# Kernel tuning notes

Hardware: AMD Instinct MI355X
Metric: run time of the kernel (lower is better)

The kernel has to match this reference:

```python
import jax, jax.numpy as jnp
import numpy as np

B, L, C = 64, 64, 16          # batch, seq_len, chars per word
V, CV = 100000, 100           # word vocab, char vocab
EMB, CHD = 300, 64            # word emb dim, char emb dim
N_HIGHWAY, N_ATTN = 2, 2
D = EMB + 3 * 50              # highway_dim = 450


def setup_inputs() -> dict:
    ks = jax.random.split(jax.random.key(0), 16)
    word_emb = jax.random.normal(ks[6], (V, EMB), jnp.float32) * 0.01
    word_emb = word_emb.at[0].set(0.0)  # padding_idx row zeroed
    return {
        "q1": jax.random.randint(ks[0], (B, L), 0, V),
        "q2": jax.random.randint(ks[1], (B, L), 0, V),
        "q1_len": jax.random.randint(ks[2], (B,), 1, L + 1),
        "q2_len": jax.random.randint(ks[3], (B,), 1, L + 1),
        "q1_char": jax.random.randint(ks[4], (B, L, C), 0, CV),
        "q2_char": jax.random.randint(ks[5], (B, L, C), 0, CV),
        "word_emb": word_emb,
        "char_emb": jax.random.normal(ks[7], (CV, CHD), jnp.float32) * 0.1,
        "conv_w3": jax.random.normal(ks[8], (50, CHD, 3), jnp.float32) / np.sqrt(CHD * 3),
        "conv_b3": jnp.zeros((50,), jnp.float32),
        "conv_w4": jax.random.normal(ks[9], (50, CHD, 4), jnp.float32) / np.sqrt(CHD * 4),
        "conv_b4": jnp.zeros((50,), jnp.float32),
        "conv_w5": jax.random.normal(ks[10], (50, CHD, 5), jnp.float32) / np.sqrt(CHD * 5),
        "conv_b5": jnp.zeros((50,), jnp.float32),
        "hw_w": jax.random.normal(ks[11], (D, D), jnp.float32) / np.sqrt(D),
        "hw_b": jnp.zeros((D,), jnp.float32),
        "attn_w": jax.random.normal(ks[12], (N_ATTN, 3 * D), jnp.float32) / np.sqrt(3 * D),
        "attn_b": jnp.zeros((N_ATTN,), jnp.float32),
    }


def _char_features(qc, emb, convs):
    # qc: [B, T, C] int -> [B, T, 150]
    Bq, T, Cc = qc.shape
    e = emb[qc.reshape(-1, Cc)].transpose(0, 2, 1)  # [B*T, CHD, C]
    outs = []
    for w, b in convs:
        h = jax.lax.conv_general_dilated(e, w, (1,), 'VALID',
                                         dimension_numbers=('NCH', 'OIH', 'NCH'))
        h = jax.nn.relu(h + b[None, :, None])
        outs.append(jnp.max(h, axis=2))  # max over char positions
    return jnp.concatenate(outs, axis=-1).reshape(Bq, T, -1)


def _highway(x, w, b):
    # NB: original reuses the SAME linear for transform and gate (bug-faithful)
    y = x @ w.T + b
    g = jax.nn.sigmoid(y)
    return g * jax.nn.relu(y) + (1.0 - g) * x


def _self_attn(x, mask, w, b):
    # Exact decomposition of Linear(concat(x_i, x_j, x_i*x_j)) -> scalar:
    # score[b,i,j] = x_i.w1 + x_j.w2 + sum_d x_i x_j w3 + b
    d = x.shape[-1]
    w1, w2, w3 = w[:d], w[d:2 * d], w[2 * d:]
    scores = ((x @ w1)[:, :, None] + (x @ w2)[:, None, :]
              + jnp.einsum('bid,bjd->bij', x * w3, x) + b)
    # original masked_fill uses -1e-09 (not -1e9) -- reproduce faithfully
    logits = jnp.where(mask[:, None, :], scores, jnp.float32(-1e-9))
    attn = jax.nn.softmax(logits, axis=-1)
    return jnp.einsum('bij,bjd->bid', attn, x)


def _branch(q, q_char, q_len, word_emb, char_emb, convs, hw_w, hw_b, attn_w, attn_b):
    mask = jnp.arange(L)[None, :] < q_len[:, None]
    x = jnp.concatenate([word_emb[q], _char_features(q_char, char_emb, convs)], axis=-1)
    for _ in range(N_HIGHWAY):
        x = _highway(x, hw_w, hw_b)
    att = x
    for i in range(N_ATTN):
        att = _self_attn(x, mask, attn_w[i], attn_b[i])
        x = att + x
    return att


def reference(q1, q2, q1_len, q2_len, q1_char, q2_char, word_emb, char_emb,
              conv_w3, conv_b3, conv_w4, conv_b4, conv_w5, conv_b5,
              hw_w, hw_b, attn_w, attn_b):
    convs = [(conv_w3, conv_b3), (conv_w4, conv_b4), (conv_w5, conv_b5)]
    a1 = _branch(q1, q1_char, q1_len, word_emb, char_emb, convs, hw_w, hw_b, attn_w, attn_b)
    a2 = _branch(q2, q2_char, q2_len, word_emb, char_emb, convs, hw_w, hw_b, attn_w, attn_b)
    return (a1, a2)
```

## Files before the change

### kernel.cpp

```cpp
#include <hip/hip_runtime.h>
#include <math.h>

#define B   64
#define L   64
#define C   16
#define CHD 64
#define EMB 300
#define D   450
#define DP  480
#define NT  (B*L)
#define NBH 128

typedef short bf16x8 __attribute__((ext_vector_type(8)));
typedef float f32x4  __attribute__((ext_vector_type(4)));
typedef float f32x2  __attribute__((ext_vector_type(2)));
typedef unsigned short ushort_t;
typedef ushort_t us4 __attribute__((ext_vector_type(4)));

#define MFMA16 __builtin_amdgcn_mfma_f32_16x16x32_bf16

#define WPF_N (10 * 10 * 512)
#define WBF_N (32 * 15 * 512)
#define XFRAG 30720

__device__ inline float wave_sum(float v) {
#pragma unroll
    for (int o = 32; o; o >>= 1) v += __shfl_xor(v, o, 64);
    return v;
}
__device__ inline ushort_t f2b(float f) {
    union { float f; unsigned u; } c; c.f = f;
    unsigned r = c.u + 0x7FFFu + ((c.u >> 16) & 1u);
    return (ushort_t)(r >> 16);
}

__global__ __launch_bounds__(256) void prep_kernel(
    const float* __restrict__ W,
    const float* __restrict__ w3, const float* __restrict__ b3,
    const float* __restrict__ w4, const float* __restrict__ b4,
    const float* __restrict__ w5, const float* __restrict__ b5,
    const float* __restrict__ char_emb,
    ushort_t* __restrict__ Wb16F, ushort_t* __restrict__ WpadF,
    float* __restrict__ bias160, ushort_t* __restrict__ ceb16)
{
    int idx = blockIdx.x * 256 + threadIdx.x;
    if (idx < WBF_N) {
        const int e = idx & 7, l = (idx >> 3) & 63, t = idx >> 9;
        const int ks = t % 15, nt = t / 15;
        const int ln = l & 15, q = l >> 4;
        const int n = nt * 16 + ln, k = ks * 32 + q * 8 + e;
        float v = (n < D && k < D) ? W[(size_t)n * D + k] : 0.f;
        Wb16F[idx] = f2b(v);
        return;
    }
    idx -= WBF_N;
    if (idx < WPF_N) {
        const int e = idx & 7, l = (idx >> 3) & 63, t = idx >> 9;
        const int ks = t % 10, nt = t / 10;
        const int ln = l & 15, q = l >> 4;
        const int f = nt * 16 + ln;
        const int kd = ks * 32 + q * 8 + e;
        const int k = kd >> 6, d = kd & 63;
        float v = 0.f;
        if (f < 50)       { if (k < 3) v = w3[f * 192 + d * 3 + k]; }
        else if (f < 100) { if (k < 4) v = w4[(f - 50) * 256 + d * 4 + k]; }
        else if (f < 150) { v = w5[(f - 100) * 320 + d * 5 + k]; }
        WpadF[idx] = f2b(v);
        return;
    }
    idx -= WPF_N;
    if (idx < 160) {
        bias160[idx] = (idx < 50) ? b3[idx] : (idx < 100) ? b4[idx - 50]
                     : (idx < 150) ? b5[idx - 100] : 0.f;
    } else if (idx < 160 + 100 * 64) {
        int i = idx - 160;
        ceb16[i] = f2b(char_emb[i]);
    }
}

#define ESS 72
#define EST (20 * ESS)
#define XTS1 488

__global__ __launch_bounds__(256) void embed_conv_kernel(
    const int* __restrict__ q1, const int* __restrict__ q2,
    const int* __restrict__ q1c, const int* __restrict__ q2c,
    const float* __restrict__ word_emb, const ushort_t* __restrict__ ceb16,
    const ushort_t* __restrict__ WpadF, const float* __restrict__ bias160,
    float* __restrict__ xout, ushort_t* __restrict__ xbF)
{
    __shared__ ushort_t es[8 * EST];
    __shared__ ushort_t Xt[8 * XTS1];

    const int tid  = threadIdx.x;
    const int wv   = tid >> 6;
    const int lane = tid & 63;
    const int ln   = lane & 15, quad = lane >> 4;
    const int bx   = blockIdx.x;
    const int tokbase = ((bx & 7) * 128 + (bx >> 3)) * 8;

#pragma unroll
    for (int i = 0; i < 4; ++i) {
        int c = tid + i * 256;
        int row = c >> 3, part = c & 7;
        int tl = row >> 4, cr = row & 15;
        int gtok   = tokbase + tl;
        int branch = gtok >> 12;
        int tokl   = gtok & (NT - 1);
        int cid    = (branch ? q2c : q1c)[tokl * C + cr];
        *(bf16x8*)&es[tl * EST + cr * ESS + part * 8] =
            *(const bf16x8*)&ceb16[cid * 64 + part * 8];
    }
    {
        int tl = tid >> 5, rr = (tid >> 3) & 3, part = tid & 7;
        bf16x8 z = {0, 0, 0, 0, 0, 0, 0, 0};
        *(bf16x8*)&es[tl * EST + (16 + rr) * ESS + part * 8] = z;
    }

#pragma unroll 1
    for (int c = tid; c < 8 * 75; c += 256) {
        const int t  = c / 75, d4 = c - t * 75;
        const int tok    = tokbase + t;
        const int branch = tok >> 12;
        const int tokl   = tok & (NT - 1);
        const int w      = (branch ? q2 : q1)[tokl];
        const float4 v = *(const float4*)(word_emb + (size_t)w * EMB + d4 * 4);
        float* dst = xout + (size_t)tok * D + d4 * 4;
        *(f32x2*)dst       = (f32x2){v.x, v.y};
        *(f32x2*)(dst + 2) = (f32x2){v.z, v.w};
        us4 pk = { f2b(v.x), f2b(v.y), f2b(v.z), f2b(v.w) };
        *(us4*)&Xt[t * XTS1 + d4 * 4] = pk;
    }
    if (tid < 240) {
        const int t = tid / 30, k = tid - t * 30;
        Xt[t * XTS1 + D + k] = 0;
    }
    __syncthreads();

    const int t0 = wv * 2, t1 = t0 + 1;
    f32x4 acc[2][10];
#pragma unroll
    for (int t = 0; t < 2; ++t)
#pragma unroll
        for (int nt = 0; nt < 10; ++nt) acc[t][nt] = (f32x4){0.f, 0.f, 0.f, 0.f};

#pragma unroll 1
    for (int ks = 0; ks < 10; ++ks) {
        const int kk   = ks * 32 + quad * 8;
        const int arow = kk >> 6, aoff = kk & 63;
        bf16x8 a0 = *(const bf16x8*)&es[t0 * EST + (ln + arow) * ESS + aoff];
        bf16x8 a1 = *(const bf16x8*)&es[t1 * EST + (ln + arow) * ESS + aoff];
#pragma unroll
        for (int nt = 0; nt < 10; ++nt) {
            bf16x8 bf = *(const bf16x8*)&WpadF[(size_t)((nt * 10 + ks) << 9) + lane * 8];
            acc[0][nt] = MFMA16(a0, bf, acc[0][nt], 0, 0, 0);
            acc[1][nt] = MFMA16(a1, bf, acc[1][nt], 0, 0, 0);
        }
    }
    __syncthreads();

    float* smf = (float*)es;
#pragma unroll
    for (int t = 0; t < 2; ++t) {
        const int tloc = t0 + t;
#pragma unroll
        for (int nt = 0; nt < 10; ++nt) {
            const int f  = nt * 16 + ln;
            const int Pf = (f < 50) ? 14 : (f < 100) ? 13 : 12;
            float m = -1e30f;
#pragma unroll
            for (int r = 0; r < 4; ++r) {
                const int p = quad * 4 + r;
                if (p < Pf) m = fmaxf(m, acc[t][nt][r]);
            }
            m = fmaxf(m, __shfl_xor(m, 16, 64));
            m = fmaxf(m, __shfl_xor(m, 32, 64));
            if (quad == 0) smf[tloc * 160 + f] = fmaxf(0.f, m + bias160[f]);
        }
    }
    __syncthreads();
#pragma unroll 1
    for (int c = tid; c < 8 * 150; c += 256) {
        const int t = c / 150, f = c - t * 150;
        const float rv = smf[t * 160 + f];
        xout[(size_t)(tokbase + t) * D + EMB + f] = rv;
        Xt[t * XTS1 + EMB + f] = f2b(rv);
    }
    __syncthreads();

    {
        const int tile = tokbase >> 4, half = (tokbase >> 3) & 1;
#pragma unroll 1
        for (int c = tid; c < 480; c += 256) {
            const int ksl = c >> 5, s = c & 31;
            const int q = s >> 3, tl = s & 7;
            const int l = q * 16 + half * 8 + tl;
            bf16x8 v = *(const bf16x8*)&Xt[tl * XTS1 + ksl * 32 + q * 8];
            *(bf16x8*)&xbF[((size_t)(tile * 15 + ksl) * 64 + l) * 8] = v;
        }
    }
}

#define HLS 72

__global__ __launch_bounds__(256, 4) void highway_mfma_kernel(
    const ushort_t* __restrict__ xbFi, const float* __restrict__ xf32,
    const ushort_t* __restrict__ Wb16F, const float* __restrict__ bvec,
    float* __restrict__ out, ushort_t* __restrict__ xbFo)
{
    __shared__ ushort_t Xl[64 * HLS];

    const int bx = blockIdx.x;
    const int cx = bx & 7, rr = bx >> 3;
    const int my = cx * 16 + (rr & 15);
    const int mx = rr >> 4;

    const int tid  = threadIdx.x;
    const int wv   = tid >> 6;
    const int lane = tid & 63;
    const int wm = wv >> 1, wn = wv & 1;
    const int m0 = my * 64 + wm * 32;
    const int n0 = mx * 64 + wn * 32;
    const int lm = lane & 15, quad = lane >> 4;

    const int tA0 = my * 4 + wm * 2;
    const ushort_t* ax0 = xbFi + (size_t)(tA0 * 15) * 512 + lane * 8;
    const ushort_t* ax1 = ax0 + 15 * 512;
    const int ntg0 = mx * 4 + wn * 2;
    const ushort_t* bw0 = Wb16F + (size_t)(ntg0 * 15) * 512 + lane * 8;
    const ushort_t* bw1 = bw0 + 15 * 512;

    f32x4 acc[2][2];
#pragma unroll
    for (int i = 0; i < 2; ++i)
#pragma unroll
        for (int j = 0; j < 2; ++j) acc[i][j] = (f32x4){0.f, 0.f, 0.f, 0.f};

#pragma unroll 3
    for (int ks = 0; ks < 15; ++ks) {
        bf16x8 a0 = *(const bf16x8*)(ax0 + ks * 512);
        bf16x8 a1 = *(const bf16x8*)(ax1 + ks * 512);
        bf16x8 b0 = *(const bf16x8*)(bw0 + ks * 512);
        bf16x8 b1 = *(const bf16x8*)(bw1 + ks * 512);
        acc[0][0] = MFMA16(a0, b0, acc[0][0], 0, 0, 0);
        acc[0][1] = MFMA16(a0, b1, acc[0][1], 0, 0, 0);
        acc[1][0] = MFMA16(a1, b0, acc[1][0], 0, 0, 0);
        acc[1][1] = MFMA16(a1, b1, acc[1][1], 0, 0, 0);
    }

#pragma unroll
    for (int nt = 0; nt < 2; ++nt) {
        const int n  = n0 + nt * 16 + lm;
        const int nl = wn * 32 + nt * 16 + lm;
        const bool nval = (n < D);
        const float bv = nval ? bvec[n] : 0.f;
#pragma unroll
        for (int mt = 0; mt < 2; ++mt) {
#pragma unroll
            for (int r = 0; r < 4; ++r) {
                const int m  = m0 + mt * 16 + quad * 4 + r;
                const int ml = wm * 32 + mt * 16 + quad * 4 + r;
                float y = acc[mt][nt][r] + bv;
                float g = 1.f / (1.f + __expf(-y));
                float o = 0.f;
                if (nval) {
                    float xo = xf32[(size_t)m * D + n];
                    o = g * fmaxf(y, 0.f) + (1.f - g) * xo;
                    out[(size_t)m * D + n] = o;
                }
                Xl[ml * HLS + nl] = f2b(nval ? o : 0.f);
            }
        }
    }
    __syncthreads();

#pragma unroll 1
    for (int c = tid; c < 512; c += 256) {
        const int fi = c >> 6, l = c & 63;
        const int tl = fi >> 1, ksl = fi & 1;
        const int ksg = mx * 2 + ksl;
        if (ksg < 15) {
            const int lnp = l & 15, qp = l >> 4;
            bf16x8 v = *(const bf16x8*)&Xl[(tl * 16 + lnp) * HLS + ksl * 32 + qp * 8];
            *(bf16x8*)&xbFo[((size_t)((my * 4 + tl) * 15 + ksg) * 64 + l) * 8] = v;
        }
    }
}

#define PXS 496

__global__ __launch_bounds__(256) void attn_prep_kernel(
    const float* __restrict__ xf32, const float* __restrict__ attn_w, int layer,
    ushort_t* __restrict__ xw3F, ushort_t* __restrict__ xTF,
    float* __restrict__ s1g, float* __restrict__ s2g)
{
    __shared__ ushort_t Xs[16 * PXS];
    __shared__ ushort_t Xw3s[16 * PXS];

    const int bx  = blockIdx.x;
    const int wid = (bx & 7) * 64 + (bx >> 3);
    const int bh  = wid >> 2, jq = wid & 3;
    const int tid = threadIdx.x;
    const int wv  = tid >> 6;
    const int lane = tid & 63;
    const size_t tok0 = (size_t)bh * 64 + jq * 16;

    const float* wb = attn_w + (size_t)layer * 3 * D;
    const float* w3 = wb + 2 * D;

#pragma unroll 1
    for (int c = tid; c < 16 * 60; c += 256) {
        const int j  = c / 60, k8 = c - j * 60;
        const int k0 = k8 * 8;
        const float* xr = xf32 + (tok0 + j) * D;
        bf16x8 xv, pv;
#pragma unroll
        for (int t = 0; t < 8; ++t) {
            const int k = k0 + t;
            const float x = (k < D) ? xr[k] : 0.f;
            xv[t] = (short)f2b(x);
            pv[t] = (short)f2b((k < D) ? x * w3[k] : 0.f);
        }
        *(bf16x8*)&Xs[j * PXS + k0]   = xv;
        *(bf16x8*)&Xw3s[j * PXS + k0] = pv;
    }

#pragma unroll 1
    for (int rr = 0; rr < 4; ++rr) {
        const int j = wv * 4 + rr;
        const float* xr = xf32 + (tok0 + j) * D;
        float a1 = 0.f, a2 = 0.f;
#pragma unroll
        for (int t = 0; t < 8; ++t) {
            const int k = lane + t * 64;
            if (k < D) {
                float xv = xr[k];
                a1 = fmaf(xv, wb[k], a1);
                a2 = fmaf(xv, wb[D + k], a2);
            }
        }
        a1 = wave_sum(a1);
        a2 = wave_sum(a2);
        if (lane == 0) { s1g[tok0 + j] = a1; s2g[tok0 + j] = a2; }
    }
    __syncthreads();

#pragma unroll 1
    for (int c = tid; c < 960; c += 256) {
        const int ks = c >> 6, l = c & 63;
        const int lnp = l & 15, qp = l >> 4;
        bf16x8 w = *(const bf16x8*)&Xw3s[lnp * PXS + ks * 32 + qp * 8];
        *(bf16x8*)&xw3F[(size_t)bh * XFRAG + ((jq * 15 + ks) * 64 + l) * 8] = w;
    }

    {
        const int half = jq >> 1, q0 = (jq & 1) * 2;
#pragma unroll 1
        for (int c = tid; c < 960; c += 256) {
            const int dt = c >> 5, s = c & 31;
            const int qp = q0 + (s >> 4), lnp = s & 15;
            const int d  = dt * 16 + lnp;
            const int jb = (qp & 1) * 8;
            bf16x8 v;
#pragma unroll
            for (int e = 0; e < 8; ++e) v[e] = (short)Xs[(jb + e) * PXS + d];
            *(bf16x8*)&xTF[(size_t)bh * XFRAG + ((dt * 2 + half) * 64 + qp * 16 + lnp) * 8] = v;
        }
    }
}

#define ALS 72

template <bool RES_EMIT>
__global__ __launch_bounds__(256) void attn_fused_kernel(
    const float* __restrict__ xf32,
    const ushort_t* __restrict__ xF, const ushort_t* __restrict__ xw3F,
    const ushort_t* __restrict__ xTF,
    const float* __restrict__ s1g, const float* __restrict__ s2g,
    const int* __restrict__ q1_len, const int* __restrict__ q2_len,
    const float* __restrict__ attn_b, int layer,
    float* __restrict__ outf, ushort_t* __restrict__ xbFo)
{
    __shared__ float    sc[16][68];
    __shared__ ushort_t Al[16 * ALS];
    __shared__ ushort_t At[RES_EMIT ? 16 * XTS1 : 8];

    const int bx  = blockIdx.x;
    const int wid = (bx & 7) * 64 + (bx >> 3);
    const int bh  = wid >> 2, iq = wid & 3;
    const int branch = bh >> 6, b = bh & 63;
    const int tid  = threadIdx.x;
    const int wv   = tid >> 6;
    const int lane = tid & 63;
    const int ln   = lane & 15, quad = lane >> 4;
    const int i0   = iq * 16;

    if (RES_EMIT) {
        for (int c = tid; c < 480; c += 256) {
            const int t = c / 30, k = c - t * 30;
            At[t * XTS1 + D + k] = 0;
        }
    }

    const ushort_t* xa = xF   + (size_t)bh * XFRAG + (iq * 15 * 64 + lane) * 8;
    const ushort_t* xb = xw3F + (size_t)bh * XFRAG + (wv * 15 * 64 + lane) * 8;

    f32x4 qa0 = (f32x4){0.f, 0.f, 0.f, 0.f};
    f32x4 qa1 = (f32x4){0.f, 0.f, 0.f, 0.f};
#pragma unroll
    for (int ks = 0; ks < 14; ks += 2) {
        bf16x8 a0 = *(const bf16x8*)(xa + ks * 512);
        bf16x8 b0 = *(const bf16x8*)(xb + ks * 512);
        bf16x8 a1 = *(const bf16x8*)(xa + ks * 512 + 512);
        bf16x8 b1 = *(const bf16x8*)(xb + ks * 512 + 512);
        qa0 = MFMA16(a0, b0, qa0, 0, 0, 0);
        qa1 = MFMA16(a1, b1, qa1, 0, 0, 0);
    }
    {
        bf16x8 a  = *(const bf16x8*)(xa + 14 * 512);
        bf16x8 bq = *(const bf16x8*)(xb + 14 * 512);
        qa0 = MFMA16(a, bq, qa0, 0, 0, 0);
    }
    f32x4 qacc = qa0 + qa1;

    const int   len  = (branch ? q2_len : q1_len)[b];
    const float bias = attn_b[layer];
    const int   j    = wv * 16 + ln;
    const float s2v  = s2g[bh * 64 + j];
#pragma unroll
    for (int reg = 0; reg < 4; ++reg) {
        const int i = i0 + quad * 4 + reg;
        float v = qacc[reg] + s1g[bh * 64 + i] + s2v + bias;
        if (j >= len) v = -1e-9f;
        sc[quad * 4 + reg][j] = v;
    }
    __syncthreads();

#pragma unroll
    for (int rr = 0; rr < 4; ++rr) {
        const int r = wv * 4 + rr;
        float v = sc[r][lane];
        float m = v;
#pragma unroll
        for (int o = 32; o; o >>= 1) m = fmaxf(m, __shfl_xor(m, o, 64));
        float ev = __expf(v - m);
        float sm = ev;
#pragma unroll
        for (int o = 32; o; o >>= 1) sm += __shfl_xor(sm, o, 64);
        Al[r * ALS + lane] = f2b(ev * (1.f / sm));
    }
    __syncthreads();

    const ushort_t* xTb = xTF + (size_t)bh * XFRAG + lane * 8;
    bf16x8 af0 = *(const bf16x8*)&Al[ln * ALS + quad * 8];
    bf16x8 af1 = *(const bf16x8*)&Al[ln * ALS + quad * 8 + 32];

#pragma unroll 2
    for (int dt = wv; dt < 30; dt += 4) {
        bf16x8 b0 = *(const bf16x8*)(xTb + dt * 1024);
        bf16x8 b1 = *(const bf16x8*)(xTb + dt * 1024 + 512);
        f32x4 acc = (f32x4){0.f, 0.f, 0.f, 0.f};
        acc = MFMA16(af0, b0, acc, 0, 0, 0);
        acc = MFMA16(af1, b1, acc, 0, 0, 0);

        const int d = dt * 16 + ln;
        if (d < D) {
#pragma unroll
            for (int reg = 0; reg < 4; ++reg) {
                const int i = i0 + quad * 4 + reg;
                float v = acc[reg];
                if (RES_EMIT) v += xf32[((size_t)bh * 64 + i) * D + d];
                outf[((size_t)bh * 64 + i) * D + d] = v;
                if (RES_EMIT)
                    At[(quad * 4 + reg) * XTS1 + d] = f2b(v);
            }
        }
    }

    if (RES_EMIT) {
        __syncthreads();
#pragma unroll 1
        for (int c = tid; c < 960; c += 256) {
            const int ksl = c >> 6, l = c & 63;
            const int lnp = l & 15, qp = l >> 4;
            bf16x8 v = *(const bf16x8*)&At[lnp * XTS1 + ksl * 32 + qp * 8];
            *(bf16x8*)&xbFo[((size_t)((bh * 4 + iq) * 15 + ksl) * 64 + l) * 8] = v;
        }
    }
}

extern "C" void kernel_launch(void* const* d_in, const int* in_sizes, int n_in,
                              void* d_out, int out_size, void* d_ws, size_t ws_size,
                              hipStream_t stream) {
    const int*   q1       = (const int*)  d_in[0];
    const int*   q2       = (const int*)  d_in[1];
    const int*   q1_len   = (const int*)  d_in[2];
    const int*   q2_len   = (const int*)  d_in[3];
    const int*   q1c      = (const int*)  d_in[4];
    const int*   q2c      = (const int*)  d_in[5];
    const float* word_emb = (const float*)d_in[6];
    const float* char_emb = (const float*)d_in[7];
    const float* w3       = (const float*)d_in[8];
    const float* b3       = (const float*)d_in[9];
    const float* w4       = (const float*)d_in[10];
    const float* b4       = (const float*)d_in[11];
    const float* w5       = (const float*)d_in[12];
    const float* b5       = (const float*)d_in[13];
    const float* hw_w     = (const float*)d_in[14];
    const float* hw_b     = (const float*)d_in[15];
    const float* attn_w   = (const float*)d_in[16];
    const float* attn_b   = (const float*)d_in[17];
    float* out = (float*)d_out;

    float*    buf0    = (float*)d_ws;
    float*    buf1    = buf0 + (size_t)2 * NT * D;
    float*    bias160 = buf1 + (size_t)2 * NT * D;
    ushort_t* xbFa    = (ushort_t*)(bias160 + 160);
    ushort_t* xbFb    = xbFa + (size_t)2 * NT * DP;
    ushort_t* Wb16F   = xbFb + (size_t)2 * NT * DP;
    ushort_t* WpadF   = Wb16F + (size_t)WBF_N;
    ushort_t* ceb16   = WpadF + (size_t)WPF_N;
    ushort_t* xw3F    = ceb16 + (size_t)100 * 64;
    ushort_t* xTF     = xw3F + (size_t)NBH * XFRAG;
    float*    s1g     = (float*)(xTF + (size_t)NBH * XFRAG);
    float*    s2g     = s1g + (size_t)2 * NT;

    prep_kernel<<<(WBF_N + WPF_N + 160 + 100 * 64 + 255) / 256, 256, 0, stream>>>(
        hw_w, w3, b3, w4, b4, w5, b5, char_emb, Wb16F, WpadF, bias160, ceb16);
    embed_conv_kernel<<<1024, 256, 0, stream>>>(q1, q2, q1c, q2c, word_emb, ceb16,
                                                WpadF, bias160, buf0, xbFa);

    highway_mfma_kernel<<<1024, 256, 0, stream>>>(xbFa, buf0, Wb16F, hw_b, buf1, xbFb);
    highway_mfma_kernel<<<1024, 256, 0, stream>>>(xbFb, buf1, Wb16F, hw_b, buf0, xbFa);

    attn_prep_kernel<<<512, 256, 0, stream>>>(buf0, attn_w, 0, xw3F, xTF, s1g, s2g);
    attn_fused_kernel<true><<<512, 256, 0, stream>>>(
        buf0, xbFa, xw3F, xTF, s1g, s2g, q1_len, q2_len, attn_b, 0, buf1, xbFb);

    attn_prep_kernel<<<512, 256, 0, stream>>>(buf1, attn_w, 1, xw3F, xTF, s1g, s2g);
    attn_fused_kernel<false><<<512, 256, 0, stream>>>(
        buf1, xbFb, xw3F, xTF, s1g, s2g, q1_len, q2_len, attn_b, 1, out, nullptr);
}
```

Measured before the change: 323.3 us.

## Fuse second highway with attention prep and attention layer with next prep

Merges the second highway layer with the layer-0 attention preparation (s1/s2 dot products, x*w3 and transposed fragments), and merges layer-0 attention with layer-1 preparation. This cuts the launch count from 7 to 5 and removes fp32 activation round-trips through global memory between kernels. In exchange the fused highway kernel runs only 512 blocks and each wave does 8 N-tiles over the full K, so it has less parallelism than the 1024-block highway kernel. It also uses more shared memory for the fp32 staging buffers.

```diff
diff --git a/kernel.cpp b/kernel.cpp
--- a/kernel.cpp
+++ b/kernel.cpp
@@ -22,6 +22,9 @@
 #define WPF_N (10 * 10 * 512)
 #define WBF_N (32 * 15 * 512)
 #define XFRAG 30720
+
+#define XFS 456
+#define XSS 488
 
 __device__ inline float wave_sum(float v) {
 #pragma unroll
@@ -80,7 +83,6 @@
 
 #define ESS 72
 #define EST (20 * ESS)
-#define XTS1 488
 
 __global__ __launch_bounds__(256) void embed_conv_kernel(
     const int* __restrict__ q1, const int* __restrict__ q2,
@@ -90,7 +92,7 @@
     float* __restrict__ xout, ushort_t* __restrict__ xbF)
 {
     __shared__ ushort_t es[8 * EST];
-    __shared__ ushort_t Xt[8 * XTS1];
+    __shared__ ushort_t Xt[8 * XSS];
 
     const int tid  = threadIdx.x;
     const int wv   = tid >> 6;
@@ -129,11 +131,11 @@
         *(f32x2*)dst       = (f32x2){v.x, v.y};
         *(f32x2*)(dst + 2) = (f32x2){v.z, v.w};
         us4 pk = { f2b(v.x), f2b(v.y), f2b(v.z), f2b(v.w) };
-        *(us4*)&Xt[t * XTS1 + d4 * 4] = pk;
+        *(us4*)&Xt[t * XSS + d4 * 4] = pk;
     }
     if (tid < 240) {
         const int t = tid / 30, k = tid - t * 30;
-        Xt[t * XTS1 + D + k] = 0;
+        Xt[t * XSS + D + k] = 0;
     }
     __syncthreads();
 
@@ -184,7 +186,7 @@
         const int t = c / 150, f = c - t * 150;
         const float rv = smf[t * 160 + f];
         xout[(size_t)(tokbase + t) * D + EMB + f] = rv;
-        Xt[t * XTS1 + EMB + f] = f2b(rv);
+        Xt[t * XSS + EMB + f] = f2b(rv);
     }
     __syncthreads();
 
@@ -195,7 +197,7 @@
             const int ksl = c >> 5, s = c & 31;
             const int q = s >> 3, tl = s & 7;
             const int l = q * 16 + half * 8 + tl;
-            bf16x8 v = *(const bf16x8*)&Xt[tl * XTS1 + ksl * 32 + q * 8];
+            bf16x8 v = *(const bf16x8*)&Xt[tl * XSS + ksl * 32 + q * 8];
             *(bf16x8*)&xbF[((size_t)(tile * 15 + ksl) * 64 + l) * 8] = v;
         }
     }
@@ -287,70 +289,108 @@
     }
 }
 
-#define PXS 496
-
-__global__ __launch_bounds__(256) void attn_prep_kernel(
-    const float* __restrict__ xf32, const float* __restrict__ attn_w, int layer,
+__global__ __launch_bounds__(256) void highway2_prep_kernel(
+    const ushort_t* __restrict__ xbFi, const float* __restrict__ xf32in,
+    const ushort_t* __restrict__ Wb16F, const float* __restrict__ bvec,
+    const float* __restrict__ attn_w,
+    float* __restrict__ outf, ushort_t* __restrict__ xbFo,
     ushort_t* __restrict__ xw3F, ushort_t* __restrict__ xTF,
     float* __restrict__ s1g, float* __restrict__ s2g)
 {
-    __shared__ ushort_t Xs[16 * PXS];
-    __shared__ ushort_t Xw3s[16 * PXS];
+    __shared__ float    Xf[16 * XFS];
+    __shared__ ushort_t Xs[16 * XSS];
 
     const int bx  = blockIdx.x;
     const int wid = (bx & 7) * 64 + (bx >> 3);
     const int bh  = wid >> 2, jq = wid & 3;
+    const int tt  = wid;
+    const int m0  = tt * 16;
     const int tid = threadIdx.x;
     const int wv  = tid >> 6;
     const int lane = tid & 63;
-    const size_t tok0 = (size_t)bh * 64 + jq * 16;
-
-    const float* wb = attn_w + (size_t)layer * 3 * D;
+    const int ln = lane & 15, quad = lane >> 4;
+
+    if (tid < 480) {
+        const int t = tid / 30, k = tid - t * 30;
+        Xs[t * XSS + D + k] = 0;
+    }
+
+    const ushort_t* ax = xbFi + (size_t)(tt * 15) * 512 + lane * 8;
+    f32x4 acc[8];
+#pragma unroll
+    for (int t = 0; t < 8; ++t) acc[t] = (f32x4){0.f, 0.f, 0.f, 0.f};
+
+#pragma unroll 1
+    for (int ks = 0; ks < 15; ++ks) {
+        bf16x8 a = *(const bf16x8*)(ax + ks * 512);
+#pragma unroll
+        for (int t = 0; t < 8; ++t) {
+            const int nt = wv * 8 + t;
+            if (nt < 30) {
+                bf16x8 b = *(const bf16x8*)&Wb16F[(size_t)(nt * 15 + ks) * 512 + lane * 8];
+                acc[t] = MFMA16(a, b, acc[t], 0, 0, 0);
+            }
+        }
+    }
+
+#pragma unroll
+    for (int t = 0; t < 8; ++t) {
+        const int nt = wv * 8 + t;
+        if (nt >= 30) continue;
+        const int n = nt * 16 + ln;
+        const bool nval = (n < D);
+        const float bv = nval ? bvec[n] : 0.f;
+#pragma unroll
+        for (int reg = 0; reg < 4; ++reg) {
+            const int i = quad * 4 + reg;
+            float y = acc[t][reg] + bv;
+            float g = 1.f / (1.f + __expf(-y));
+            if (nval) {
+                float xo = xf32in[(size_t)(m0 + i) * D + n];
+                float o = g * fmaxf(y, 0.f) + (1.f - g) * xo;
+                outf[(size_t)(m0 + i) * D + n] = o;
+                Xf[i * XFS + n] = o;
+                Xs[i * XSS + n] = f2b(o);
+            }
+        }
+    }
+    __syncthreads();
+
+    const float* wb = attn_w;
     const float* w3 = wb + 2 * D;
-
-#pragma unroll 1
-    for (int c = tid; c < 16 * 60; c += 256) {
-        const int j  = c / 60, k8 = c - j * 60;
-        const int k0 = k8 * 8;
-        const float* xr = xf32 + (tok0 + j) * D;
-        bf16x8 xv, pv;
-#pragma unroll
-        for (int t = 0; t < 8; ++t) {
-            const int k = k0 + t;
-            const float x = (k < D) ? xr[k] : 0.f;
-            xv[t] = (short)f2b(x);
-            pv[t] = (short)f2b((k < D) ? x * w3[k] : 0.f);
-        }
-        *(bf16x8*)&Xs[j * PXS + k0]   = xv;
-        *(bf16x8*)&Xw3s[j * PXS + k0] = pv;
-    }
 
 #pragma unroll 1
     for (int rr = 0; rr < 4; ++rr) {
         const int j = wv * 4 + rr;
-        const float* xr = xf32 + (tok0 + j) * D;
         float a1 = 0.f, a2 = 0.f;
 #pragma unroll
         for (int t = 0; t < 8; ++t) {
             const int k = lane + t * 64;
             if (k < D) {
-                float xv = xr[k];
+                float xv = Xf[j * XFS + k];
                 a1 = fmaf(xv, wb[k], a1);
                 a2 = fmaf(xv, wb[D + k], a2);
             }
         }
         a1 = wave_sum(a1);
         a2 = wave_sum(a2);
-        if (lane == 0) { s1g[tok0 + j] = a1; s2g[tok0 + j] = a2; }
-    }
-    __syncthreads();
+        if (lane == 0) { s1g[m0 + j] = a1; s2g[m0 + j] = a2; }
+    }
 
 #pragma unroll 1
     for (int c = tid; c < 960; c += 256) {
         const int ks = c >> 6, l = c & 63;
         const int lnp = l & 15, qp = l >> 4;
-        bf16x8 w = *(const bf16x8*)&Xw3s[lnp * PXS + ks * 32 + qp * 8];
-        *(bf16x8*)&xw3F[(size_t)bh * XFRAG + ((jq * 15 + ks) * 64 + l) * 8] = w;
+        bf16x8 v = *(const bf16x8*)&Xs[lnp * XSS + ks * 32 + qp * 8];
+        *(bf16x8*)&xbFo[((size_t)(tt * 15 + ks) * 64 + l) * 8] = v;
+        bf16x8 pv;
+#pragma unroll
+        for (int e = 0; e < 8; ++e) {
+            const int k = ks * 32 + qp * 8 + e;
+            const float x = (k < D) ? Xf[lnp * XFS + k] : 0.f;
+            pv[e] = (short)f2b((k < D) ? x * w3[k] : 0.f);
+        }
+        *(bf16x8*)&xw3F[(size_t)bh * XFRAG + ((jq * 15 + ks) * 64 + l) * 8] = pv;
     }
 
     {
@@ -363,7 +403,7 @@
             const int jb = (qp & 1) * 8;
             bf16x8 v;
 #pragma unroll
-            for (int e = 0; e < 8; ++e) v[e] = (short)Xs[(jb + e) * PXS + d];
+            for (int e = 0; e < 8; ++e) v[e] = (short)Xs[(jb + e) * XSS + d];
             *(bf16x8*)&xTF[(size_t)bh * XFRAG + ((dt * 2 + half) * 64 + qp * 16 + lnp) * 8] = v;
         }
     }
@@ -371,19 +411,21 @@
 
 #define ALS 72
 
-template <bool RES_EMIT>
-__global__ __launch_bounds__(256) void attn_fused_kernel(
+__global__ __launch_bounds__(256) void attn_core_prep_kernel(
     const float* __restrict__ xf32,
     const ushort_t* __restrict__ xF, const ushort_t* __restrict__ xw3F,
     const ushort_t* __restrict__ xTF,
     const float* __restrict__ s1g, const float* __restrict__ s2g,
     const int* __restrict__ q1_len, const int* __restrict__ q2_len,
-    const float* __restrict__ attn_b, int layer,
-    float* __restrict__ outf, ushort_t* __restrict__ xbFo)
+    const float* __restrict__ attn_b, const float* __restrict__ attn_w,
+    ushort_t* __restrict__ xbFo,
+    ushort_t* __restrict__ xw3Fo, ushort_t* __restrict__ xTFo,
+    float* __restrict__ s1o, float* __restrict__ s2o)
 {
     __shared__ float    sc[16][68];
     __shared__ ushort_t Al[16 * ALS];
-    __shared__ ushort_t At[RES_EMIT ? 16 * XTS1 : 8];
+    __shared__ float    Af[16 * XFS];
+    __shared__ ushort_t At[16 * XSS];
 
     const int bx  = blockIdx.x;
     const int wid = (bx & 7) * 64 + (bx >> 3);
@@ -394,12 +436,11 @@
     const int lane = tid & 63;
     const int ln   = lane & 15, quad = lane >> 4;
     const int i0   = iq * 16;
-
-    if (RES_EMIT) {
-        for (int c = tid; c < 480; c += 256) {
-            const int t = c / 30, k = c - t * 30;
-            At[t * XTS1 + D + k] = 0;
-        }
+    const int m0   = bh * 64 + i0;
+
+    if (tid < 480) {
+        const int t = tid / 30, k = tid - t * 30;
+        At[t * XSS + D + k] = 0;
     }
 
     const ushort_t* xa = xF   + (size_t)bh * XFRAG + (iq * 15 * 64 + lane) * 8;
@@ -424,7 +465,7 @@
     f32x4 qacc = qa0 + qa1;
 
     const int   len  = (branch ? q2_len : q1_len)[b];
-    const float bias = attn_b[layer];
+    const float bias = attn_b[0];
     const int   j    = wv * 16 + ln;
     const float s2v  = s2g[bh * 64 + j];
 #pragma unroll
@@ -467,24 +508,157 @@
         if (d < D) {
 #pragma unroll
             for (int reg = 0; reg < 4; ++reg) {
+                const int il = quad * 4 + reg;
+                float v = acc[reg] + xf32[(size_t)(m0 + il) * D + d];
+                Af[il * XFS + d] = v;
+                At[il * XSS + d] = f2b(v);
+            }
+        }
+    }
+    __syncthreads();
+
+    const float* wb1 = attn_w + 3 * D;
+    const float* w31 = wb1 + 2 * D;
+
+#pragma unroll 1
+    for (int rr = 0; rr < 4; ++rr) {
+        const int jj = wv * 4 + rr;
+        float a1 = 0.f, a2 = 0.f;
+#pragma unroll
+        for (int t = 0; t < 8; ++t) {
+            const int k = lane + t * 64;
+            if (k < D) {
+                float xv = Af[jj * XFS + k];
+                a1 = fmaf(xv, wb1[k], a1);
+                a2 = fmaf(xv, wb1[D + k], a2);
+            }
+        }
+        a1 = wave_sum(a1);
+        a2 = wave_sum(a2);
+        if (lane == 0) { s1o[m0 + jj] = a1; s2o[m0 + jj] = a2; }
+    }
+
+#pragma unroll 1
+    for (int c = tid; c < 960; c += 256) {
+        const int ks = c >> 6, l = c & 63;
+        const int lnp = l & 15, qp = l >> 4;
+        bf16x8 v = *(const bf16x8*)&At[lnp * XSS + ks * 32 + qp * 8];
+        *(bf16x8*)&xbFo[((size_t)((bh * 4 + iq) * 15 + ks) * 64 + l) * 8] = v;
+        bf16x8 pv;
+#pragma unroll
+        for (int e = 0; e < 8; ++e) {
+            const int k = ks * 32 + qp * 8 + e;
+            const float x = (k < D) ? Af[lnp * XFS + k] : 0.f;
+            pv[e] = (short)f2b((k < D) ? x * w31[k] : 0.f);
+        }
+        *(bf16x8*)&xw3Fo[(size_t)bh * XFRAG + ((iq * 15 + ks) * 64 + l) * 8] = pv;
+    }
+
+    {
+        const int half = iq >> 1, q0 = (iq & 1) * 2;
+#pragma unroll 1
+        for (int c = tid; c < 960; c += 256) {
+            const int dt = c >> 5, s = c & 31;
+            const int qp = q0 + (s >> 4), lnp = s & 15;
+            const int d  = dt * 16 + lnp;
+            const int jb = (qp & 1) * 8;
+            bf16x8 v;
+#pragma unroll
+            for (int e = 0; e < 8; ++e) v[e] = (short)At[(jb + e) * XSS + d];
+            *(bf16x8*)&xTFo[(size_t)bh * XFRAG + ((dt * 2 + half) * 64 + qp * 16 + lnp) * 8] = v;
+        }
+    }
+}
+
+__global__ __launch_bounds__(256) void attn_core_final_kernel(
+    const ushort_t* __restrict__ xF, const ushort_t* __restrict__ xw3F,
+    const ushort_t* __restrict__ xTF,
+    const float* __restrict__ s1g, const float* __restrict__ s2g,
+    const int* __restrict__ q1_len, const int* __restrict__ q2_len,
+    const float* __restrict__ attn_b,
+    float* __restrict__ outf)
+{
+    __shared__ float    sc[16][68];
+    __shared__ ushort_t Al[16 * ALS];
+
+    const int bx  = blockIdx.x;
+    const int wid = (bx & 7) * 64 + (bx >> 3);
+    const int bh  = wid >> 2, iq = wid & 3;
+    const int branch = bh >> 6, b = bh & 63;
+    const int tid  = threadIdx.x;
+    const int wv   = tid >> 6;
+    const int lane = tid & 63;
+    const int ln   = lane & 15, quad = lane >> 4;
+    const int i0   = iq * 16;
+
+    const ushort_t* xa = xF   + (size_t)bh * XFRAG + (iq * 15 * 64 + lane) * 8;
+    const ushort_t* xb = xw3F + (size_t)bh * XFRAG + (wv * 15 * 64 + lane) * 8;
+
+    f32x4 qa0 = (f32x4){0.f, 0.f, 0.f, 0.f};
+    f32x4 qa1 = (f32x4){0.f, 0.f, 0.f, 0.f};
+#pragma unroll
+    for (int ks = 0; ks < 14; ks += 2) {
+        bf16x8 a0 = *(const bf16x8*)(xa + ks * 512);
+        bf16x8 b0 = *(const bf16x8*)(xb + ks * 512);
+        bf16x8 a1 = *(const bf16x8*)(xa + ks * 512 + 512);
+        bf16x8 b1 = *(const bf16x8*)(xb + ks * 512 + 512);
+        qa0 = MFMA16(a0, b0, qa0, 0, 0, 0);
+        qa1 = MFMA16(a1, b1, qa1, 0, 0, 0);
+    }
+    {
+        bf16x8 a  = *(const bf16x8*)(xa + 14 * 512);
+        bf16x8 bq = *(const bf16x8*)(xb + 14 * 512);
+        qa0 = MFMA16(a, bq, qa0, 0, 0, 0);
+    }
+    f32x4 qacc = qa0 + qa1;
+
+    const int   len  = (branch ? q2_len : q1_len)[b];
+    const float bias = attn_b[1];
+    const int   j    = wv * 16 + ln;
+    const float s2v  = s2g[bh * 64 + j];
+#pragma unroll
+    for (int reg = 0; reg < 4; ++reg) {
+        const int i = i0 + quad * 4 + reg;
+        float v = qacc[reg] + s1g[bh * 64 + i] + s2v + bias;
+        if (j >= len) v = -1e-9f;
+        sc[quad * 4 + reg][j] = v;
+    }
+    __syncthreads();
+
+#pragma unroll
+    for (int rr = 0; rr < 4; ++rr) {
+        const int r = wv * 4 + rr;
+        float v = sc[r][lane];
+        float m = v;
+#pragma unroll
+        for (int o = 32; o; o >>= 1) m = fmaxf(m, __shfl_xor(m, o, 64));
+        float ev = __expf(v - m);
+        float sm = ev;
+#pragma unroll
+        for (int o = 32; o; o >>= 1) sm += __shfl_xor(sm, o, 64);
+        Al[r * ALS + lane] = f2b(ev * (1.f / sm));
+    }
+    __syncthreads();
+
+    const ushort_t* xTb = xTF + (size_t)bh * XFRAG + lane * 8;
+    bf16x8 af0 = *(const bf16x8*)&Al[ln * ALS + quad * 8];
+    bf16x8 af1 = *(const bf16x8*)&Al[ln * ALS + quad * 8 + 32];
+
+#pragma unroll 2
+    for (int dt = wv; dt < 30; dt += 4) {
+        bf16x8 b0 = *(const bf16x8*)(xTb + dt * 1024);
+        bf16x8 b1 = *(const bf16x8*)(xTb + dt * 1024 + 512);
+        f32x4 acc = (f32x4){0.f, 0.f, 0.f, 0.f};
+        acc = MFMA16(af0, b0, acc, 0, 0, 0);
+        acc = MFMA16(af1, b1, acc, 0, 0, 0);
+
+        const int d = dt * 16 + ln;
+        if (d < D) {
+#pragma unroll
+            for (int reg = 0; reg < 4; ++reg) {
                 const int i = i0 + quad * 4 + reg;
-                float v = acc[reg];
-                if (RES_EMIT) v += xf32[((size_t)bh * 64 + i) * D + d];
-                outf[((size_t)bh * 64 + i) * D + d] = v;
-                if (RES_EMIT)
-                    At[(quad * 4 + reg) * XTS1 + d] = f2b(v);
+                outf[((size_t)bh * 64 + i) * D + d] = acc[reg];
             }
-        }
-    }
-
-    if (RES_EMIT) {
-        __syncthreads();
-#pragma unroll 1
-        for (int c = tid; c < 960; c += 256) {
-            const int ksl = c >> 6, l = c & 63;
-            const int lnp = l & 15, qp = l >> 4;
-            bf16x8 v = *(const bf16x8*)&At[lnp * XTS1 + ksl * 32 + qp * 8];
-            *(bf16x8*)&xbFo[((size_t)((bh * 4 + iq) * 15 + ksl) * 64 + l) * 8] = v;
         }
     }
 }
@@ -520,10 +694,14 @@
     ushort_t* Wb16F   = xbFb + (size_t)2 * NT * DP;
     ushort_t* WpadF   = Wb16F + (size_t)WBF_N;
     ushort_t* ceb16   = WpadF + (size_t)WPF_N;
-    ushort_t* xw3F    = ceb16 + (size_t)100 * 64;
-    ushort_t* xTF     = xw3F + (size_t)NBH * XFRAG;
-    float*    s1g     = (float*)(xTF + (size_t)NBH * XFRAG);
-    float*    s2g     = s1g + (size_t)2 * NT;
+    ushort_t* xw3Fa   = ceb16 + (size_t)100 * 64;
+    ushort_t* xTFa    = xw3Fa + (size_t)NBH * XFRAG;
+    ushort_t* xw3Fb   = xTFa  + (size_t)NBH * XFRAG;
+    ushort_t* xTFb    = xw3Fb + (size_t)NBH * XFRAG;
+    float*    s1a     = (float*)(xTFb + (size_t)NBH * XFRAG);
+    float*    s2a     = s1a + (size_t)2 * NT;
+    float*    s1b     = s2a + (size_t)2 * NT;
+    float*    s2b     = s1b + (size_t)2 * NT;
 
     prep_kernel<<<(WBF_N + WPF_N + 160 + 100 * 64 + 255) / 256, 256, 0, stream>>>(
         hw_w, w3, b3, w4, b4, w5, b5, char_emb, Wb16F, WpadF, bias160, ceb16);
@@ -531,13 +709,14 @@
                                                 WpadF, bias160, buf0, xbFa);
 
     highway_mfma_kernel<<<1024, 256, 0, stream>>>(xbFa, buf0, Wb16F, hw_b, buf1, xbFb);
-    highway_mfma_kernel<<<1024, 256, 0, stream>>>(xbFb, buf1, Wb16F, hw_b, buf0, xbFa);
-
-    attn_prep_kernel<<<512, 256, 0, stream>>>(buf0, attn_w, 0, xw3F, xTF, s1g, s2g);
-    attn_fused_kernel<true><<<512, 256, 0, stream>>>(
-        buf0, xbFa, xw3F, xTF, s1g, s2g, q1_len, q2_len, attn_b, 0, buf1, xbFb);
-
-    attn_prep_kernel<<<512, 256, 0, stream>>>(buf1, attn_w, 1, xw3F, xTF, s1g, s2g);
-    attn_fused_kernel<false><<<512, 256, 0, stream>>>(
-        buf1, xbFb, xw3F, xTF, s1g, s2g, q1_len, q2_len, attn_b, 1, out, nullptr);
-}
+
+    highway2_prep_kernel<<<512, 256, 0, stream>>>(
+        xbFb, buf1, Wb16F, hw_b, attn_w, buf0, xbFa, xw3Fa, xTFa, s1a, s2a);
+
+    attn_core_prep_kernel<<<512, 256, 0, stream>>>(
+        buf0, xbFa, xw3Fa, xTFa, s1a, s2a, q1_len, q2_len, attn_b, attn_w,
+        xbFb, xw3Fb, xTFb, s1b, s2b);
+
+    attn_core_final_kernel<<<512, 256, 0, stream>>>(
+        xbFb, xw3Fb, xTFb, s1b, s2b, q1_len, q2_len, attn_b, out);
+}
```

Result: no change. 324.0 us (+0.2%).
